# Performance work log

Measured on AMD Instinct MI355X. Metric: run time of the kernel, lower is better.

Reference implementation:

```python
import jax, jax.numpy as jnp
import numpy as np

NUM_GRAPHS = 1024  # fill_max for batch ids; fixed num_segments for jit


def setup_inputs() -> dict:
    key = jax.random.key(0)
    k1, k2 = jax.random.split(key)
    N, D = 1000000, 256
    x = jax.random.normal(k1, (N, D), dtype=jnp.float32)
    batch = jnp.sort(jax.random.randint(k2, (N,), 0, NUM_GRAPHS, dtype=jnp.int64))
    return {"input": x, "batch": batch}


def reference(input, batch):
    # per-node L2 norm over feature dim: [N]
    all_norms = jnp.sqrt(jnp.sum(input.astype(jnp.float32) ** 2, axis=1))
    seg = batch.astype(jnp.int32)
    # segment-reduce: sum of norms and node counts per graph, [NUM_GRAPHS]
    norm_sum = jax.ops.segment_sum(all_norms, seg, num_segments=NUM_GRAPHS)
    counts = jax.ops.segment_sum(jnp.ones_like(all_norms), seg, num_segments=NUM_GRAPHS)
    per_graph = jnp.where(counts > 0, norm_sum / counts, 0.0)
    # original loops b in range(batch.max()) -> graphs 0..max-1 only
    bmax = batch.max().astype(jnp.float32)
    mask = jnp.arange(NUM_GRAPHS, dtype=jnp.float32) < bmax
    norm_mean = jnp.sum(per_graph * mask) / (bmax + 1.0)
    # module returns input unchanged; norm_mean is the recorded statistic
    return input, norm_mean
```

## Files before the change

kernel.cpp:

```cpp
#include <hip/hip_runtime.h>

#define NUM_GRAPHS 1024
#define D 256

typedef float f4 __attribute__((ext_vector_type(4)));

__global__ void activs_init_kernel(float* __restrict__ sums, float* __restrict__ cnts) {
    int i = blockIdx.x * blockDim.x + threadIdx.x;
    if (i < NUM_GRAPHS) {
        sums[i] = 0.0f;
        cnts[i] = 0.0f;
    }
}

__global__ __launch_bounds__(256) void activs_main_kernel(
        const float* __restrict__ x, const int* __restrict__ batch,
        float* __restrict__ out, float* __restrict__ sums,
        float* __restrict__ cnts, int N) {
    const int lane = threadIdx.x & 63;
    const int waveId = (blockIdx.x * blockDim.x + threadIdx.x) >> 6;
    const int totalWaves = (gridDim.x * blockDim.x) >> 6;

    const int rowsPerWave = (N + totalWaves - 1) / totalWaves;
    const int r0 = waveId * rowsPerWave;
    const int r1 = min(r0 + rowsPerWave, N);

    float runSum = 0.0f;
    float runCnt = 0.0f;
    int curSeg = -1;

    int r = r0;
    for (; r + 1 < r1; r += 2) {
        const f4* src0 = (const f4*)(x + (size_t)r * D) + lane;
        const f4* src1 = (const f4*)(x + (size_t)(r + 1) * D) + lane;
        f4 v0 = __builtin_nontemporal_load(src0);
        f4 v1 = __builtin_nontemporal_load(src1);
        __builtin_nontemporal_store(v0, (f4*)(out + (size_t)r * D) + lane);
        __builtin_nontemporal_store(v1, (f4*)(out + (size_t)(r + 1) * D) + lane);

        float s0 = v0.x * v0.x + v0.y * v0.y + v0.z * v0.z + v0.w * v0.w;
        float s1 = v1.x * v1.x + v1.y * v1.y + v1.z * v1.z + v1.w * v1.w;
        #pragma unroll
        for (int m = 32; m; m >>= 1) {
            s0 += __shfl_xor(s0, m, 64);
            s1 += __shfl_xor(s1, m, 64);
        }

        if (lane == 0) {
            int seg0 = batch[r];
            int seg1 = batch[r + 1];
            if (seg0 != curSeg) {
                if (runCnt > 0.0f) {
                    atomicAdd(&sums[curSeg], runSum);
                    atomicAdd(&cnts[curSeg], runCnt);
                }
                curSeg = seg0;
                runSum = 0.0f;
                runCnt = 0.0f;
            }
            runSum += sqrtf(s0);
            runCnt += 1.0f;
            if (seg1 != curSeg) {
                atomicAdd(&sums[curSeg], runSum);
                atomicAdd(&cnts[curSeg], runCnt);
                curSeg = seg1;
                runSum = 0.0f;
                runCnt = 0.0f;
            }
            runSum += sqrtf(s1);
            runCnt += 1.0f;
        }
    }
    if (r < r1) {
        const f4* src = (const f4*)(x + (size_t)r * D) + lane;
        f4 v = __builtin_nontemporal_load(src);
        __builtin_nontemporal_store(v, (f4*)(out + (size_t)r * D) + lane);
        float s = v.x * v.x + v.y * v.y + v.z * v.z + v.w * v.w;
        #pragma unroll
        for (int m = 32; m; m >>= 1) s += __shfl_xor(s, m, 64);
        if (lane == 0) {
            int seg = batch[r];
            if (seg != curSeg) {
                if (runCnt > 0.0f) {
                    atomicAdd(&sums[curSeg], runSum);
                    atomicAdd(&cnts[curSeg], runCnt);
                }
                curSeg = seg;
                runSum = 0.0f;
                runCnt = 0.0f;
            }
            runSum += sqrtf(s);
            runCnt += 1.0f;
        }
    }
    if (lane == 0 && runCnt > 0.0f) {
        atomicAdd(&sums[curSeg], runSum);
        atomicAdd(&cnts[curSeg], runCnt);
    }
}

__global__ __launch_bounds__(1024) void activs_finalize_kernel(
        const float* __restrict__ sums, const float* __restrict__ cnts,
        const int* __restrict__ batch, int N, float* __restrict__ out_scalar) {
    __shared__ float red[16];
    const int i = threadIdx.x;
    const int lane = i & 63;
    const int w = i >> 6;

    const float bmax = (float)batch[N - 1];

    float c = cnts[i];
    float pg = (c > 0.0f) ? (sums[i] / c) : 0.0f;
    float val = (((float)i) < bmax) ? pg : 0.0f;

    #pragma unroll
    for (int m = 32; m; m >>= 1) val += __shfl_xor(val, m, 64);
    if (lane == 0) red[w] = val;
    __syncthreads();

    if (w == 0) {
        float v = (lane < 16) ? red[lane] : 0.0f;
        #pragma unroll
        for (int m = 8; m; m >>= 1) v += __shfl_xor(v, m, 64);
        if (lane == 0) out_scalar[0] = v / (bmax + 1.0f);
    }
}

extern "C" void kernel_launch(void* const* d_in, const int* in_sizes, int n_in,
                              void* d_out, int out_size, void* d_ws, size_t ws_size,
                              hipStream_t stream) {
    const float* x = (const float*)d_in[0];
    const int* batch = (const int*)d_in[1];
    float* out = (float*)d_out;

    const int N = in_sizes[1];

    float* sums = (float*)d_ws;
    float* cnts = sums + NUM_GRAPHS;

    hipLaunchKernelGGL(activs_init_kernel, dim3(4), dim3(256), 0, stream, sums, cnts);

    hipLaunchKernelGGL(activs_main_kernel, dim3(2048), dim3(256), 0, stream,
                       x, batch, out, sums, cnts, N);

    hipLaunchKernelGGL(activs_finalize_kernel, dim3(1), dim3(1024), 0, stream,
                       sums, cnts, batch, N, out + (size_t)N * D);
}
```

Baseline: 432.4 us.

## Interleave rows across waves within each block and drop nontemporal loads/stores

Rows are now assigned per block, with the four waves in a block taking interleaved rows (stride 4), instead of each wave owning a separate contiguous chunk. This gives neighbouring waves adjacent memory, which should improve DRAM page locality and coalescing across a block. Nontemporal load and store builtins are replaced with plain float4 accesses, which changes cache behaviour for the large streaming copy. Segment runs per wave are now non-contiguous, so there may be more atomic flushes, but the batch ids are sorted and segments are long, so this stays small.

```diff
diff --git a/kernel.cpp b/kernel.cpp
--- a/kernel.cpp
+++ b/kernel.cpp
@@ -2,8 +2,6 @@
 
 #define NUM_GRAPHS 1024
 #define D 256
-
-typedef float f4 __attribute__((ext_vector_type(4)));
 
 __global__ void activs_init_kernel(float* __restrict__ sums, float* __restrict__ cnts) {
     int i = blockIdx.x * blockDim.x + threadIdx.x;
@@ -18,25 +16,24 @@
         float* __restrict__ out, float* __restrict__ sums,
         float* __restrict__ cnts, int N) {
     const int lane = threadIdx.x & 63;
-    const int waveId = (blockIdx.x * blockDim.x + threadIdx.x) >> 6;
-    const int totalWaves = (gridDim.x * blockDim.x) >> 6;
+    const int waveInBlock = threadIdx.x >> 6;
+    const int numBlocks = gridDim.x;
 
-    const int rowsPerWave = (N + totalWaves - 1) / totalWaves;
-    const int r0 = waveId * rowsPerWave;
-    const int r1 = min(r0 + rowsPerWave, N);
+    const int rowsPerBlock = (N + numBlocks - 1) / numBlocks;
+    const int rowStart = blockIdx.x * rowsPerBlock;
+    const int rowEnd = min(rowStart + rowsPerBlock, N);
 
     float runSum = 0.0f;
     float runCnt = 0.0f;
     int curSeg = -1;
 
-    int r = r0;
-    for (; r + 1 < r1; r += 2) {
-        const f4* src0 = (const f4*)(x + (size_t)r * D) + lane;
-        const f4* src1 = (const f4*)(x + (size_t)(r + 1) * D) + lane;
-        f4 v0 = __builtin_nontemporal_load(src0);
-        f4 v1 = __builtin_nontemporal_load(src1);
-        __builtin_nontemporal_store(v0, (f4*)(out + (size_t)r * D) + lane);
-        __builtin_nontemporal_store(v1, (f4*)(out + (size_t)(r + 1) * D) + lane);
+    int r = rowStart + waveInBlock;
+
+    for (; r + 4 < rowEnd; r += 8) {
+        const float4 v0 = ((const float4*)(x + (size_t)r * D))[lane];
+        const float4 v1 = ((const float4*)(x + (size_t)(r + 4) * D))[lane];
+        ((float4*)(out + (size_t)r * D))[lane] = v0;
+        ((float4*)(out + (size_t)(r + 4) * D))[lane] = v1;
 
         float s0 = v0.x * v0.x + v0.y * v0.y + v0.z * v0.z + v0.w * v0.w;
         float s1 = v1.x * v1.x + v1.y * v1.y + v1.z * v1.z + v1.w * v1.w;
@@ -47,8 +44,8 @@
         }
 
         if (lane == 0) {
-            int seg0 = batch[r];
-            int seg1 = batch[r + 1];
+            const int seg0 = batch[r];
+            const int seg1 = batch[r + 4];
             if (seg0 != curSeg) {
                 if (runCnt > 0.0f) {
                     atomicAdd(&sums[curSeg], runSum);
@@ -71,15 +68,14 @@
             runCnt += 1.0f;
         }
     }
-    if (r < r1) {
-        const f4* src = (const f4*)(x + (size_t)r * D) + lane;
-        f4 v = __builtin_nontemporal_load(src);
-        __builtin_nontemporal_store(v, (f4*)(out + (size_t)r * D) + lane);
+    for (; r < rowEnd; r += 4) {
+        const float4 v = ((const float4*)(x + (size_t)r * D))[lane];
+        ((float4*)(out + (size_t)r * D))[lane] = v;
         float s = v.x * v.x + v.y * v.y + v.z * v.z + v.w * v.w;
         #pragma unroll
         for (int m = 32; m; m >>= 1) s += __shfl_xor(s, m, 64);
         if (lane == 0) {
-            int seg = batch[r];
+            const int seg = batch[r];
             if (seg != curSeg) {
                 if (runCnt > 0.0f) {
                     atomicAdd(&sums[curSeg], runSum);
```

Measured after the change: 432.3 us. No clear change (-0.0%).
